# Optimization experiments

Hardware: AMD Instinct MI355X
Metric: run time of the kernel (lower is better)

The kernel has to match this reference:

```python
import jax, jax.numpy as jnp
import numpy as np

VOC, MEM, NSLOTS, NSENT, MAXLEN, QLEN, ANSLEN, B = 32000, 128, 20, 128, 32, 16, 8, 64


def _xavier(k, shape):
    fan_out, fan_in = shape
    std = jnp.sqrt(2.0 / (fan_in + fan_out))
    return (jax.random.normal(k, shape, jnp.float32) * std).astype(jnp.float32)


def setup_inputs() -> dict:
    key = jax.random.key(0)
    ks = jax.random.split(key, 12)
    inp = {}
    inp["input_ids"] = jax.random.randint(ks[0], (B, NSENT, MAXLEN), 0, VOC)
    inp["question"] = jax.random.randint(ks[1], (B, QLEN), 0, VOC)
    inp["ans"] = jax.random.randint(ks[2], (B, ANSLEN, 2), 0, VOC)
    E = jax.random.normal(ks[3], (VOC, MEM), jnp.float32)
    inp["E"] = E.at[0].set(0.0)  # padding_idx=0
    inp["Uw"] = _xavier(ks[4], (MEM, MEM)); inp["Ub"] = jnp.zeros((MEM,), jnp.float32)
    inp["Vw"] = _xavier(ks[5], (MEM, MEM)); inp["Vb"] = jnp.zeros((MEM,), jnp.float32)
    inp["Ww"] = _xavier(ks[6], (MEM, MEM)); inp["Wb"] = jnp.zeros((MEM,), jnp.float32)
    inp["slot_keys"] = jax.random.normal(ks[7], (NSLOTS, MEM), jnp.float32)  # self.w
    inp["Hw"] = _xavier(ks[8], (MEM, MEM)); inp["Hb"] = jnp.zeros((MEM,), jnp.float32)
    return inp


def reference(input_ids, question, ans, E, Uw, Ub, Vw, Vb, Ww, Wb, slot_keys, Hw, Hb):
    E0 = E.at[0].set(0.0)  # padding row stays zero
    bsz = input_ids.shape[0]
    n_sent = input_ids.shape[1]
    tok = input_ids.reshape(bsz, -1)
    # original indexes s[:, t, :] for t < n_sent over the flattened story
    s = E0[tok[:, :n_sent]]                       # [B, T, m]
    Ws = jnp.einsum('btm,nm->btn', s, Ww) + Wb    # precompute W(s_t): [B, T, m]
    Vkey = slot_keys @ Vw.T + Vb                  # [J, m]

    def step(mem, xs):
        # mem: [B, J, m]
        s_t, ws_t = xs                            # [B, m], [B, m]
        g = jax.nn.sigmoid(jnp.einsum('bm,bjm->bj', s_t, mem) + s_t @ slot_keys.T)  # [B, J]
        h_cand = jax.nn.relu(
            jnp.einsum('bjm,nm->bjn', mem, Uw) + Ub
            + Vkey[None, :, :] + ws_t[:, None, :]
        )  # dropout is identity in eval mode
        mem = mem + g[..., None] * h_cand
        # torch.norm(mem_j): global Frobenius norm over (batch, mem) per slot
        norms = jnp.sqrt(jnp.sum(mem * mem, axis=(0, 2), keepdims=True))
        return mem / norms, None

    mem0 = jnp.zeros((bsz, slot_keys.shape[0], s.shape[-1]), s.dtype)
    h, _ = jax.lax.scan(step, mem0, (jnp.swapaxes(s, 0, 1), jnp.swapaxes(Ws, 0, 1)))
    # output module
    q = E0[question].mean(1)                      # [B, m]
    a1 = E0[ans[:, :, 0]].mean(1)                 # [B, m]
    a2 = E0[ans[:, :, 1]].mean(1)                 # [B, m]
    p = jax.nn.softmax(jnp.einsum('bjm,bm->bj', h, q), axis=-1)   # [B, J]
    u = jnp.einsum('bj,bjm->bm', p, h)            # [B, m]
    r = jax.nn.relu(q + u @ Hw.T + Hb)            # [B, m]
    y1 = jnp.sum(r * a1, axis=1)
    y2 = jnp.sum(r * a2, axis=1)
    return jax.nn.softmax(jnp.stack((y1, y2), axis=1), axis=1)
```

## Files before the change

### kernel.cpp

```cpp
#include <hip/hip_runtime.h>
#include <math.h>


typedef __attribute__((ext_vector_type(8)))  short bf16x8;
typedef __attribute__((ext_vector_type(16))) float f32x16;

__device__ __forceinline__ unsigned short f2bh(float x) {
    unsigned int u = __float_as_uint(x);
    u += 0x7FFFu + ((u >> 16) & 1u);
    return (unsigned short)(u >> 16);
}
__device__ __forceinline__ float blo(unsigned int w) { return __uint_as_float(w << 16); }
__device__ __forceinline__ float bhi(unsigned int w) { return __uint_as_float(w & 0xFFFF0000u); }

__device__ __forceinline__ float dpp_xor1_add(float x) {
    int y = __builtin_amdgcn_update_dpp(0, __float_as_int(x), 0xB1, 0xF, 0xF, true);
    return x + __int_as_float(y);
}
__device__ __forceinline__ float dpp_xor2_add(float x) {
    int y = __builtin_amdgcn_update_dpp(0, __float_as_int(x), 0x4E, 0xF, 0xF, true);
    return x + __int_as_float(y);
}

#define LDS_BARRIER() do {                                   \
    asm volatile("s_waitcnt lgkmcnt(0)" ::: "memory");       \
    __builtin_amdgcn_s_barrier();                            \
    asm volatile("" ::: "memory");                           \
} while (0)

__global__ __launch_bounds__(128) void prep_kernel(
    const int* __restrict__ ids, const int* __restrict__ ques, const int* __restrict__ ans,
    const float* __restrict__ E, const float* __restrict__ Ww, const float* __restrict__ Wb,
    const float* __restrict__ Vw, const float* __restrict__ Vb, const float* __restrict__ skeys,
    float* __restrict__ sT, float* __restrict__ WsT, float* __restrict__ vkey,
    float* __restrict__ qv, float* __restrict__ a1v, float* __restrict__ a2v,
    float* __restrict__ SK)
{
    const int bi  = blockIdx.x;
    const int tid = threadIdx.x;
    __shared__ float s_l[8][132];
    __shared__ float sk_l[20 * 132];
    __shared__ float k_l[128];
    if (bi < 1024) {
        const int b = bi >> 4;
        const int g = bi & 15;
        for (int r = tid; r < 2560; r += 128) sk_l[(r >> 7) * 132 + (r & 127)] = skeys[r];
        for (int tt = 0; tt < 8; ++tt) {
            const int t     = g * 8 + tt;
            const int token = ids[b * 4096 + t];
            const float v   = E[token * 128 + tid];
            s_l[tt][tid] = v;
            sT[(t * 64 + b) * 128 + tid] = v;
        }
        __syncthreads();
        float acc[8];
        const float wbn = Wb[tid];
        #pragma unroll
        for (int i = 0; i < 8; ++i) acc[i] = wbn;
        const float4* wrow = (const float4*)(Ww + tid * 128);
        for (int m4 = 0; m4 < 32; ++m4) {
            const float4 w = wrow[m4];
            #pragma unroll
            for (int tt = 0; tt < 8; ++tt) {
                acc[tt] += s_l[tt][m4*4+0]*w.x + s_l[tt][m4*4+1]*w.y
                         + s_l[tt][m4*4+2]*w.z + s_l[tt][m4*4+3]*w.w;
            }
        }
        for (int tt = 0; tt < 8; ++tt)
            WsT[((g*8+tt) * 64 + b) * 128 + tid] = acc[tt];
        for (int idx = tid; idx < 160; idx += 128) {
            const int tt = idx / 20;
            const int jj = idx - tt * 20;
            float d = 0.f;
            for (int m = 0; m < 128; ++m) d += s_l[tt][m] * sk_l[jj * 132 + m];
            SK[(jj * 128 + (g*8 + tt)) * 64 + b] = d;
        }
    } else if (bi < 1044) {
        const int j = bi - 1024;
        k_l[tid] = skeys[j * 128 + tid];
        __syncthreads();
        float acc = Vb[tid];
        const float4* vrow = (const float4*)(Vw + tid * 128);
        for (int m4 = 0; m4 < 32; ++m4) {
            const float4 w = vrow[m4];
            acc += k_l[m4*4]*w.x + k_l[m4*4+1]*w.y + k_l[m4*4+2]*w.z + k_l[m4*4+3]*w.w;
        }
        vkey[j * 128 + tid] = acc;
    } else {
        const int b = bi - 1044;
        float sq = 0.f, s1 = 0.f, s2 = 0.f;
        for (int i = 0; i < 16; ++i) sq += E[ques[b*16+i] * 128 + tid];
        for (int i = 0; i < 8;  ++i) s1 += E[ans[(b*8+i)*2+0] * 128 + tid];
        for (int i = 0; i < 8;  ++i) s2 += E[ans[(b*8+i)*2+1] * 128 + tid];
        qv [b*128+tid] = sq * (1.f/16.f);
        a1v[b*128+tid] = s1 * 0.125f;
        a2v[b*128+tid] = s2 * 0.125f;
    }
}

__global__ __launch_bounds__(512, 1) void scan_kernel(
    const float* __restrict__ sT, const float* __restrict__ WsT,
    const float* __restrict__ vkey, const float* __restrict__ Uw,
    const float* __restrict__ Ub, const float* __restrict__ SK,
    float* __restrict__ h_out)
{
    __shared__ unsigned short AB[64 * 136];
    __shared__ float g_l[64];
    __shared__ float wred[8];

    const int j    = blockIdx.x;
    const int tid  = threadIdx.x;
    const int wave = tid >> 6;
    const int lane = tid & 63;
    const int l32  = lane & 31;
    const int q    = lane >> 5;
    const int bt2  = wave & 1;
    const int nt2  = wave >> 1;
    const int n    = nt2 * 32 + l32;
    const int gb   = tid >> 3;
    const int gm   = (tid & 7) * 16;

    bf16x8 b_h[8];
    {
        const int k0 = q * 8;
        #pragma unroll
        for (int kc = 0; kc < 8; ++kc) {
            const float4* src = (const float4*)(Uw + n * 128 + kc * 16 + k0);
            const float4 v0 = src[0], v1 = src[1];
            const float xs[8] = {v0.x,v0.y,v0.z,v0.w, v1.x,v1.y,v1.z,v1.w};
            #pragma unroll
            for (int e = 0; e < 8; ++e) b_h[kc][e] = (short)f2bh(xs[e]);
        }
    }
    for (int i = tid; i < 64 * 136 / 2; i += 512) ((unsigned int*)AB)[i] = 0u;
    const float ubv = Ub[n] + vkey[j * 128 + n];

    unsigned woffB[16];
    #pragma unroll
    for (int r = 0; r < 16; ++r) {
        const int brow = bt2*32 + 4*q + (r & 3) + 8*(r >> 2);
        woffB[r] = (unsigned)((brow * 128 + n) * 4);
    }
    const unsigned soffB = (unsigned)((gb * 128 + gm) * 4);
    const unsigned koffB = (unsigned)(gb * 4);
    const char* SKj = (const char*)SK + (size_t)j * 32768;

    float xprev[16];
    #pragma unroll
    for (int r = 0; r < 16; ++r) xprev[r] = 0.f;

    float4 svA0, svA1, svA2, svA3, svB0, svB1, svB2, svB3;
    float  skvA, skvB;
    float  wsv[16];
    {
        const float4* s4 = (const float4*)((const char*)sT + soffB);
        svA0 = s4[0]; svA1 = s4[1]; svA2 = s4[2]; svA3 = s4[3];
        skvA = *(const float*)(SKj + koffB);
        const char* pW = (const char*)WsT;
        #pragma unroll
        for (int r = 0; r < 16; ++r) wsv[r] = *(const float*)(pW + woffB[r]);
    }
    __syncthreads();

    float inv_s = 1.f;

#define SCAN_STEP(T_CUR, Sc0,Sc1,Sc2,Sc3,SKc, Sn0,Sn1,Sn2,Sn3,SKn)             \
    {                                                                          \
        const int tn = (T_CUR < 127) ? (T_CUR) + 1 : 127;                      \
                        \
        {                                                                      \
            const float4* s4 = (const float4*)((const char*)sT + (size_t)tn * 32768 + soffB); \
            Sn0 = s4[0]; Sn1 = s4[1]; Sn2 = s4[2]; Sn3 = s4[3];                \
            SKn = *(const float*)(SKj + (size_t)tn * 256 + koffB);             \
        }                                                                      \
               \
        {                                                                      \
            const uint4* u4 = (const uint4*)(AB + gb * 136 + gm);              \
            const uint4 w0 = u4[0], w1 = u4[1];                                \
            float a0 = Sc0.x*blo(w0.x), a1 = Sc0.y*bhi(w0.x);                  \
            float a2 = Sc0.z*blo(w0.y), a3 = Sc0.w*bhi(w0.y);                  \
            a0 = fmaf(Sc1.x, blo(w0.z), a0); a1 = fmaf(Sc1.y, bhi(w0.z), a1);  \
            a2 = fmaf(Sc1.z, blo(w0.w), a2); a3 = fmaf(Sc1.w, bhi(w0.w), a3);  \
            a0 = fmaf(Sc2.x, blo(w1.x), a0); a1 = fmaf(Sc2.y, bhi(w1.x), a1);  \
            a2 = fmaf(Sc2.z, blo(w1.y), a2); a3 = fmaf(Sc2.w, bhi(w1.y), a3);  \
            a0 = fmaf(Sc3.x, blo(w1.z), a0); a1 = fmaf(Sc3.y, bhi(w1.z), a1);  \
            a2 = fmaf(Sc3.z, blo(w1.w), a2); a3 = fmaf(Sc3.w, bhi(w1.w), a3);  \
            float d1 = (a0 + a1) + (a2 + a3);                                  \
            d1 = dpp_xor1_add(d1);                                             \
            d1 = dpp_xor2_add(d1);                                             \
            d1 += __shfl_xor(d1, 4, 64);                                       \
            if ((tid & 7) == 0) {                                              \
                const float e = __expf(-(inv_s * d1 + SKc));                   \
                g_l[gb] = __builtin_amdgcn_rcpf(1.f + e);                      \
            }                                                                  \
        }                                                                      \
                         \
        f32x16 acc0 = {0.f,0.f,0.f,0.f,0.f,0.f,0.f,0.f,                        \
                       0.f,0.f,0.f,0.f,0.f,0.f,0.f,0.f};                       \
        f32x16 acc1 = acc0;                                                    \
        {                                                                      \
            const unsigned short* arow = AB + (bt2*32 + l32) * 136 + q * 8;    \
            _Pragma("unroll")                                                  \
            for (int kc = 0; kc < 8; ++kc) {                                   \
                const bf16x8 a = *(const bf16x8*)(arow + kc * 16);             \
                if (kc & 1) acc1 = __builtin_amdgcn_mfma_f32_32x32x16_bf16(a, b_h[kc], acc1, 0, 0, 0); \
                else        acc0 = __builtin_amdgcn_mfma_f32_32x32x16_bf16(a, b_h[kc], acc0, 0, 0, 0); \
            }                                                                  \
            acc0 += acc1;      \
        }                                                                      \
        LDS_BARRIER();                 \
                                    \
        const float4 gA = *(const float4*)(g_l + bt2*32 + 4*q + 0);            \
        const float4 gB = *(const float4*)(g_l + bt2*32 + 4*q + 8);            \
        const float4 gC = *(const float4*)(g_l + bt2*32 + 4*q + 16);           \
        const float4 gD = *(const float4*)(g_l + bt2*32 + 4*q + 24);           \
        const float gr[16] = {gA.x,gA.y,gA.z,gA.w, gB.x,gB.y,gB.z,gB.w,        \
                              gC.x,gC.y,gC.z,gC.w, gD.x,gD.y,gD.z,gD.w};       \
        float sq0 = 0.f, sq1 = 0.f;                                            \
        _Pragma("unroll")                                                      \
        for (int r = 0; r < 16; ++r) {                                         \
            const int brow = bt2*32 + 4*q + (r & 3) + 8*(r >> 2);              \
            float hr = fmaf(inv_s, acc0[r], ubv + wsv[r]);                     \
            hr = fmaxf(hr, 0.f);                                   \
            const float x = fmaf(inv_s, xprev[r], gr[r] * hr);                 \
            xprev[r] = x;                                 \
            AB[brow*136 + n] = (unsigned short)(__float_as_uint(x) >> 16);     \
            if (r & 1) sq1 = fmaf(x, x, sq1); else sq0 = fmaf(x, x, sq0);      \
        }                                                                      \
            \
        {                                                                      \
            const char* pW = (const char*)WsT + (size_t)tn * 32768;            \
            _Pragma("unroll")                                                  \
            for (int r = 0; r < 16; ++r)                                       \
                wsv[r] = *(const float*)(pW + woffB[r]);                       \
        }                                                                      \
        float ssq = sq0 + sq1;                                                 \
        ssq = dpp_xor1_add(ssq);                                               \
        ssq = dpp_xor2_add(ssq);                                               \
        ssq += __shfl_xor(ssq, 4, 64);                                         \
        ssq += __shfl_xor(ssq, 8, 64);                                         \
        ssq += __shfl_xor(ssq, 16, 64);                                        \
        ssq += __shfl_xor(ssq, 32, 64);                                        \
        if (lane == 0) wred[wave] = ssq;                                       \
        LDS_BARRIER();     \
        const float4 w0 = *(const float4*)(wred);                              \
        const float4 w1 = *(const float4*)(wred + 4);                          \
        inv_s = __builtin_amdgcn_rsqf(w0.x+w0.y+w0.z+w0.w + w1.x+w1.y+w1.z+w1.w); \
    }

    for (int t = 0; t < 128; t += 2) {
        SCAN_STEP(t,     svA0,svA1,svA2,svA3,skvA, svB0,svB1,svB2,svB3,skvB)
        SCAN_STEP(t + 1, svB0,svB1,svB2,svB3,skvB, svA0,svA1,svA2,svA3,skvA)
    }
#undef SCAN_STEP

    #pragma unroll
    for (int r = 0; r < 16; ++r) {
        const int brow = bt2*32 + 4*q + (r & 3) + 8*(r >> 2);
        h_out[(brow*20 + j)*128 + n] = inv_s * xprev[r];
    }
}

__global__ __launch_bounds__(128) void final_kernel(
    const float* __restrict__ h, const float* __restrict__ qv,
    const float* __restrict__ a1v, const float* __restrict__ a2v,
    const float* __restrict__ Hw, const float* __restrict__ Hb,
    float* __restrict__ out)
{
    const int b   = blockIdx.x;
    const int tid = threadIdx.x;
    __shared__ float hb[20][128];
    __shared__ float ql[128];
    __shared__ float ul[128];
    __shared__ float pl[20];
    __shared__ float lgt[20];
    __shared__ float red1[2], red2[2];

    for (int jj = 0; jj < 20; ++jj) hb[jj][tid] = h[(b*20+jj)*128 + tid];
    ql[tid] = qv[b*128 + tid];
    __syncthreads();
    if (tid < 20) {
        float d = 0.f;
        for (int m = 0; m < 128; ++m) d += hb[tid][m] * ql[m];
        lgt[tid] = d;
    }
    __syncthreads();
    if (tid == 0) {
        float mx = lgt[0];
        for (int jj = 1; jj < 20; ++jj) mx = fmaxf(mx, lgt[jj]);
        float s = 0.f;
        for (int jj = 0; jj < 20; ++jj) { const float e = expf(lgt[jj]-mx); pl[jj] = e; s += e; }
        const float is = 1.f / s;
        for (int jj = 0; jj < 20; ++jj) pl[jj] *= is;
    }
    __syncthreads();
    float u = 0.f;
    for (int jj = 0; jj < 20; ++jj) u += pl[jj] * hb[jj][tid];
    ul[tid] = u;
    __syncthreads();
    float acc = ql[tid] + Hb[tid];
    const float4* hwr = (const float4*)(Hw + tid*128);
    for (int m4 = 0; m4 < 32; ++m4) {
        const float4 w = hwr[m4];
        acc += ul[m4*4]*w.x + ul[m4*4+1]*w.y + ul[m4*4+2]*w.z + ul[m4*4+3]*w.w;
    }
    const float r  = fmaxf(acc, 0.f);
    float y1 = r * a1v[b*128+tid];
    float y2 = r * a2v[b*128+tid];
    #pragma unroll
    for (int mask = 1; mask < 64; mask <<= 1) {
        y1 += __shfl_xor(y1, mask, 64);
        y2 += __shfl_xor(y2, mask, 64);
    }
    if ((tid & 63) == 0) { red1[tid>>6] = y1; red2[tid>>6] = y2; }
    __syncthreads();
    if (tid == 0) {
        const float z1 = red1[0] + red1[1];
        const float z2 = red2[0] + red2[1];
        const float mx = fmaxf(z1, z2);
        const float e1 = expf(z1-mx), e2 = expf(z2-mx);
        const float s  = e1 + e2;
        out[b*2+0] = e1 / s;
        out[b*2+1] = e2 / s;
    }
}

extern "C" void kernel_launch(void* const* d_in, const int* in_sizes, int n_in,
                              void* d_out, int out_size, void* d_ws, size_t ws_size,
                              hipStream_t stream)
{
    const int*   ids  = (const int*)  d_in[0];
    const int*   ques = (const int*)  d_in[1];
    const int*   ans  = (const int*)  d_in[2];
    const float* E    = (const float*)d_in[3];
    const float* Uw   = (const float*)d_in[4];
    const float* Ubv  = (const float*)d_in[5];
    const float* Vw   = (const float*)d_in[6];
    const float* Vb   = (const float*)d_in[7];
    const float* Ww   = (const float*)d_in[8];
    const float* Wb   = (const float*)d_in[9];
    const float* sk   = (const float*)d_in[10];
    const float* Hw   = (const float*)d_in[11];
    const float* Hb   = (const float*)d_in[12];

    float* ws   = (float*)d_ws;
    float* sT   = ws;
    float* WsT  = sT  + 1048576;
    float* vkey = WsT + 1048576;
    float* qv   = vkey + 2560;
    float* a1v  = qv  + 8192;
    float* a2v  = a1v + 8192;
    float* h    = a2v + 8192;
    float* SK   = h   + 163840;

    prep_kernel<<<1108, 128, 0, stream>>>(ids, ques, ans, E, Ww, Wb, Vw, Vb, sk,
                                          sT, WsT, vkey, qv, a1v, a2v, SK);
    scan_kernel<<<20, 512, 0, stream>>>(sT, WsT, vkey, Uw, Ubv, SK, h);
    final_kernel<<<64, 128, 0, stream>>>(h, qv, a1v, a2v, Hw, Hb, (float*)d_out);
}
```

Baseline: 293.0 us.

## Store story embeddings as bf16 and compute gate dot with fdot2 reusing MFMA operands

The prep kernel now writes the per-step story embeddings in bf16, in a chunked layout suited to row-per-lane access. The scan kernel's gate dot product (s_t · mem) moves to two waves that each own a batch row. It uses v_dot2 bf16 instructions on the same LDS row fragments that are then reused as MFMA A operands, which removes a duplicate LDS read and the 8-lane shuffle reduction. This halves the story bandwidth and shortens the per-step serial path, at the cost of bf16 rounding on s_t and load imbalance, since only 2 of 8 waves do the gate work.

Measured after the change: 429.2 us. 46.5% more time.

```diff
diff --git a/kernel.cpp b/kernel.cpp
--- a/kernel.cpp
+++ b/kernel.cpp
@@ -12,6 +12,18 @@
 }
 __device__ __forceinline__ float blo(unsigned int w) { return __uint_as_float(w << 16); }
 __device__ __forceinline__ float bhi(unsigned int w) { return __uint_as_float(w & 0xFFFF0000u); }
+
+#if __has_builtin(__builtin_amdgcn_fdot2_f32_bf16)
+typedef __attribute__((ext_vector_type(2))) __bf16 bf16x2v;
+__device__ __forceinline__ float dot2bf(unsigned int a, unsigned int b, float c) {
+    return __builtin_amdgcn_fdot2_f32_bf16(
+        __builtin_bit_cast(bf16x2v, a), __builtin_bit_cast(bf16x2v, b), c, false);
+}
+#else
+__device__ __forceinline__ float dot2bf(unsigned int a, unsigned int b, float c) {
+    return fmaf(bhi(a), bhi(b), fmaf(blo(a), blo(b), c));
+}
+#endif
 
 __device__ __forceinline__ float dpp_xor1_add(float x) {
     int y = __builtin_amdgcn_update_dpp(0, __float_as_int(x), 0xB1, 0xF, 0xF, true);
@@ -32,7 +44,7 @@
     const int* __restrict__ ids, const int* __restrict__ ques, const int* __restrict__ ans,
     const float* __restrict__ E, const float* __restrict__ Ww, const float* __restrict__ Wb,
     const float* __restrict__ Vw, const float* __restrict__ Vb, const float* __restrict__ skeys,
-    float* __restrict__ sT, float* __restrict__ WsT, float* __restrict__ vkey,
+    unsigned short* __restrict__ sT2, float* __restrict__ WsT, float* __restrict__ vkey,
     float* __restrict__ qv, float* __restrict__ a1v, float* __restrict__ a2v,
     float* __restrict__ SK)
 {
@@ -45,12 +57,14 @@
         const int b = bi >> 4;
         const int g = bi & 15;
         for (int r = tid; r < 2560; r += 128) sk_l[(r >> 7) * 132 + (r & 127)] = skeys[r];
+        const int chunk = tid >> 3;
+        const int elem  = tid & 7;
         for (int tt = 0; tt < 8; ++tt) {
             const int t     = g * 8 + tt;
             const int token = ids[b * 4096 + t];
             const float v   = E[token * 128 + tid];
             s_l[tt][tid] = v;
-            sT[(t * 64 + b) * 128 + tid] = v;
+            sT2[((t * 16 + chunk) * 64 + b) * 8 + elem] = f2bh(v);
         }
         __syncthreads();
         float acc[8];
@@ -99,7 +113,7 @@
 }
 
 __global__ __launch_bounds__(512, 1) void scan_kernel(
-    const float* __restrict__ sT, const float* __restrict__ WsT,
+    const unsigned short* __restrict__ sT2, const float* __restrict__ WsT,
     const float* __restrict__ vkey, const float* __restrict__ Uw,
     const float* __restrict__ Ub, const float* __restrict__ SK,
     float* __restrict__ h_out)
@@ -117,8 +131,7 @@
     const int bt2  = wave & 1;
     const int nt2  = wave >> 1;
     const int n    = nt2 * 32 + l32;
-    const int gb   = tid >> 3;
-    const int gm   = (tid & 7) * 16;
+    const int brow0= bt2 * 32 + l32;
 
     bf16x8 b_h[8];
     {
@@ -141,21 +154,24 @@
         const int brow = bt2*32 + 4*q + (r & 3) + 8*(r >> 2);
         woffB[r] = (unsigned)((brow * 128 + n) * 4);
     }
-    const unsigned soffB = (unsigned)((gb * 128 + gm) * 4);
-    const unsigned koffB = (unsigned)(gb * 4);
     const char* SKj = (const char*)SK + (size_t)j * 32768;
+    const char* sfb = (const char*)sT2 + (size_t)q * 1024 + (size_t)brow0 * 16;
+    const unsigned b4 = (unsigned)(brow0 * 4);
 
     float xprev[16];
     #pragma unroll
     for (int r = 0; r < 16; ++r) xprev[r] = 0.f;
 
-    float4 svA0, svA1, svA2, svA3, svB0, svB1, svB2, svB3;
-    float  skvA, skvB;
-    float  wsv[16];
+    uint4 sfA[8], sfB[8];
+    float skgA = 0.f, skgB = 0.f;
+    float wsv[16];
     {
-        const float4* s4 = (const float4*)((const char*)sT + soffB);
-        svA0 = s4[0]; svA1 = s4[1]; svA2 = s4[2]; svA3 = s4[3];
-        skvA = *(const float*)(SKj + koffB);
+        if (wave < 2) {
+            #pragma unroll
+            for (int kc = 0; kc < 8; ++kc)
+                sfA[kc] = *(const uint4*)(sfb + kc * 2048);
+            skgA = *(const float*)(SKj + b4);
+        }
         const char* pW = (const char*)WsT;
         #pragma unroll
         for (int r = 0; r < 16; ++r) wsv[r] = *(const float*)(pW + woffB[r]);
@@ -164,50 +180,51 @@
 
     float inv_s = 1.f;
 
-#define SCAN_STEP(T_CUR, Sc0,Sc1,Sc2,Sc3,SKc, Sn0,Sn1,Sn2,Sn3,SKn)             \
+#define SCAN_STEP(T_CUR, SFc, SKGc, SFn, SKGn)                                 \
     {                                                                          \
         const int tn = (T_CUR < 127) ? (T_CUR) + 1 : 127;                      \
-                        \
-        {                                                                      \
-            const float4* s4 = (const float4*)((const char*)sT + (size_t)tn * 32768 + soffB); \
-            Sn0 = s4[0]; Sn1 = s4[1]; Sn2 = s4[2]; Sn3 = s4[3];                \
-            SKn = *(const float*)(SKj + (size_t)tn * 256 + koffB);             \
-        }                                                                      \
-               \
-        {                                                                      \
-            const uint4* u4 = (const uint4*)(AB + gb * 136 + gm);              \
-            const uint4 w0 = u4[0], w1 = u4[1];                                \
-            float a0 = Sc0.x*blo(w0.x), a1 = Sc0.y*bhi(w0.x);                  \
-            float a2 = Sc0.z*blo(w0.y), a3 = Sc0.w*bhi(w0.y);                  \
-            a0 = fmaf(Sc1.x, blo(w0.z), a0); a1 = fmaf(Sc1.y, bhi(w0.z), a1);  \
-            a2 = fmaf(Sc1.z, blo(w0.w), a2); a3 = fmaf(Sc1.w, bhi(w0.w), a3);  \
-            a0 = fmaf(Sc2.x, blo(w1.x), a0); a1 = fmaf(Sc2.y, bhi(w1.x), a1);  \
-            a2 = fmaf(Sc2.z, blo(w1.y), a2); a3 = fmaf(Sc2.w, bhi(w1.y), a3);  \
-            a0 = fmaf(Sc3.x, blo(w1.z), a0); a1 = fmaf(Sc3.y, bhi(w1.z), a1);  \
-            a2 = fmaf(Sc3.z, blo(w1.w), a2); a3 = fmaf(Sc3.w, bhi(w1.w), a3);  \
-            float d1 = (a0 + a1) + (a2 + a3);                                  \
-            d1 = dpp_xor1_add(d1);                                             \
-            d1 = dpp_xor2_add(d1);                                             \
-            d1 += __shfl_xor(d1, 4, 64);                                       \
-            if ((tid & 7) == 0) {                                              \
-                const float e = __expf(-(inv_s * d1 + SKc));                   \
-                g_l[gb] = __builtin_amdgcn_rcpf(1.f + e);                      \
+                   \
+        if (wave < 2) {                                                        \
+            const char* pS = sfb + (size_t)tn * 16384;                         \
+            _Pragma("unroll")                                                  \
+            for (int kc = 0; kc < 8; ++kc)                                     \
+                SFn[kc] = *(const uint4*)(pS + kc * 2048);                     \
+            SKGn = *(const float*)(SKj + (size_t)tn * 256 + b4);               \
+        }                                                                      \
+                                \
+        uint4 w[8];                                                            \
+        const unsigned short* arow = AB + brow0 * 136 + q * 8;                 \
+        _Pragma("unroll")                                                      \
+        for (int kc = 0; kc < 8; ++kc)                                         \
+            w[kc] = *(const uint4*)(arow + kc * 16);                           \
+                   \
+        if (wave < 2) {                                                        \
+            float d0 = 0.f, d1 = 0.f, d2 = 0.f, d3 = 0.f;                      \
+            _Pragma("unroll")                                                  \
+            for (int kc = 0; kc < 8; ++kc) {                                   \
+                d0 = dot2bf(w[kc].x, SFc[kc].x, d0);                           \
+                d1 = dot2bf(w[kc].y, SFc[kc].y, d1);                           \
+                d2 = dot2bf(w[kc].z, SFc[kc].z, d2);                           \
+                d3 = dot2bf(w[kc].w, SFc[kc].w, d3);                           \
             }                                                                  \
-        }                                                                      \
-                         \
+            float dd = (d0 + d1) + (d2 + d3);                                  \
+            dd += __shfl_xor(dd, 32, 64);                \
+            if (q == 0) {                                                      \
+                const float e = __expf(-fmaf(inv_s, dd, SKGc));                \
+                g_l[brow0] = __builtin_amdgcn_rcpf(1.f + e);                   \
+            }                                                                  \
+        }                                                                      \
+                    \
         f32x16 acc0 = {0.f,0.f,0.f,0.f,0.f,0.f,0.f,0.f,                        \
                        0.f,0.f,0.f,0.f,0.f,0.f,0.f,0.f};                       \
         f32x16 acc1 = acc0;                                                    \
-        {                                                                      \
-            const unsigned short* arow = AB + (bt2*32 + l32) * 136 + q * 8;    \
-            _Pragma("unroll")                                                  \
-            for (int kc = 0; kc < 8; ++kc) {                                   \
-                const bf16x8 a = *(const bf16x8*)(arow + kc * 16);             \
-                if (kc & 1) acc1 = __builtin_amdgcn_mfma_f32_32x32x16_bf16(a, b_h[kc], acc1, 0, 0, 0); \
-                else        acc0 = __builtin_amdgcn_mfma_f32_32x32x16_bf16(a, b_h[kc], acc0, 0, 0, 0); \
-            }                                                                  \
-            acc0 += acc1;      \
-        }                                                                      \
+        _Pragma("unroll")                                                      \
+        for (int kc = 0; kc < 8; ++kc) {                                       \
+            const bf16x8 a = __builtin_bit_cast(bf16x8, w[kc]);                \
+            if (kc & 1) acc1 = __builtin_amdgcn_mfma_f32_32x32x16_bf16(a, b_h[kc], acc1, 0, 0, 0); \
+            else        acc0 = __builtin_amdgcn_mfma_f32_32x32x16_bf16(a, b_h[kc], acc0, 0, 0, 0); \
+        }                                                                      \
+        acc0 += acc1;                                                          \
         LDS_BARRIER();                 \
                                     \
         const float4 gA = *(const float4*)(g_l + bt2*32 + 4*q + 0);            \
@@ -249,8 +266,8 @@
     }
 
     for (int t = 0; t < 128; t += 2) {
-        SCAN_STEP(t,     svA0,svA1,svA2,svA3,skvA, svB0,svB1,svB2,svB3,skvB)
-        SCAN_STEP(t + 1, svB0,svB1,svB2,svB3,skvB, svA0,svA1,svA2,svA3,skvA)
+        SCAN_STEP(t,     sfA, skgA, sfB, skgB)
+        SCAN_STEP(t + 1, sfB, skgB, sfA, skgA)
     }
 #undef SCAN_STEP
 
@@ -344,17 +361,17 @@
     const float* Hb   = (const float*)d_in[12];
 
     float* ws   = (float*)d_ws;
-    float* sT   = ws;
-    float* WsT  = sT  + 1048576;
-    float* vkey = WsT + 1048576;
-    float* qv   = vkey + 2560;
-    float* a1v  = qv  + 8192;
-    float* a2v  = a1v + 8192;
-    float* h    = a2v + 8192;
-    float* SK   = h   + 163840;
+    unsigned short* sT2 = (unsigned short*)ws;
+    float* WsT  = ws    + 524288;
+    float* vkey = WsT   + 1048576;
+    float* qv   = vkey  + 2560;
+    float* a1v  = qv    + 8192;
+    float* a2v  = a1v   + 8192;
+    float* h    = a2v   + 8192;
+    float* SK   = h     + 163840;
 
     prep_kernel<<<1108, 128, 0, stream>>>(ids, ques, ans, E, Ww, Wb, Vw, Vb, sk,
-                                          sT, WsT, vkey, qv, a1v, a2v, SK);
-    scan_kernel<<<20, 512, 0, stream>>>(sT, WsT, vkey, Uw, Ubv, SK, h);
+                                          sT2, WsT, vkey, qv, a1v, a2v, SK);
+    scan_kernel<<<20, 512, 0, stream>>>(sT2, WsT, vkey, Uw, Ubv, SK, h);
     final_kernel<<<64, 128, 0, stream>>>(h, qv, a1v, a2v, Hw, Hb, (float*)d_out);
 }
```
